# Performance work log

Measured on AMD Instinct MI355X. Metric: run time of the kernel, lower is better.

The kernel has to match this reference:

```python
import jax, jax.numpy as jnp
import numpy as np

B, N, DIN, HID, DOUT = 1024, 128, 256, 256, 256
KDIM = 4 * N  # fcq/fck output dim = n_node * 4


def setup_inputs() -> dict:
    key = jax.random.key(0)
    ks = jax.random.split(key, 11)
    s = 0.05
    x = jax.random.normal(ks[0], (B, N, DIN), dtype=jnp.float32)
    # binary attention mask in {0,1}
    mask = jax.random.randint(ks[1], (B, N, N), 0, 2).astype(jnp.float32)
    Wv = jax.random.normal(ks[2], (DIN, HID), dtype=jnp.float32) * s
    bv = jax.random.normal(ks[3], (HID,), dtype=jnp.float32) * s
    Wq = jax.random.normal(ks[4], (DIN, KDIM), dtype=jnp.float32) * s
    bq = jax.random.normal(ks[5], (KDIM,), dtype=jnp.float32) * s
    Wk = jax.random.normal(ks[6], (DIN, KDIM), dtype=jnp.float32) * s
    bk = jax.random.normal(ks[7], (KDIM,), dtype=jnp.float32) * s
    Wo = jax.random.normal(ks[8], (HID, DOUT), dtype=jnp.float32) * s
    bo = jax.random.normal(ks[9], (DOUT,), dtype=jnp.float32) * s
    return {"x": x, "mask": mask, "Wv": Wv, "bv": bv, "Wq": Wq, "bq": bq,
            "Wk": Wk, "bk": bk, "Wo": Wo, "bo": bo}


def reference(x, mask, Wv, bv, Wq, bq, Wk, bk, Wo, bo):
    # v: [B,N,HID], q/k: [B,N,4N]
    v = jax.nn.relu(jnp.einsum('bnd,dh->bnh', x, Wv) + bv)
    q = jax.nn.relu(jnp.einsum('bnd,dk->bnk', x, Wq) + bq)
    k = jax.nn.relu(jnp.einsum('bnd,dk->bnk', x, Wk) + bk)
    # scores: bmm(q, k^T) -> [B,N,N]
    scores = jnp.einsum('bnk,bmk->bnm', q, k)
    val = scores * mask - 1000.0 * (1.0 - mask)
    att = jax.nn.softmax(val, axis=2)
    ctx = jnp.einsum('bnm,bmh->bnh', att, v)  # [B,N,HID]
    out = jax.nn.relu(jnp.einsum('bnh,hd->bnd', ctx, Wo) + bo)
    return out, att
```

## Files before the change

kernel.cpp:

```cpp
#include <hip/hip_runtime.h>
#include <cstdint>
#include <cstddef>

#define B_SZ 1024
#define N_SZ 128
#define DIN 256
#define HID 256
#define DOUT 256
#define KD 512

typedef unsigned short u16;
typedef _Float16 f16x8 __attribute__((ext_vector_type(8)));
typedef float floatx4 __attribute__((ext_vector_type(4)));
typedef unsigned short u16x8 __attribute__((ext_vector_type(8)));

#define MFMA16(a,b,c) __builtin_amdgcn_mfma_f32_16x16x32_f16(a, b, c, 0, 0, 0)

__device__ __forceinline__ u16 f2h(float f) {
    _Float16 h = (_Float16)f;
    return *(u16*)&h;
}

__device__ __forceinline__ void barx() {
    asm volatile("" ::: "memory");
    __builtin_amdgcn_s_barrier();
    asm volatile("" ::: "memory");
}
__device__ __forceinline__ void bar_lgkm() {
    asm volatile("s_waitcnt lgkmcnt(0)" ::: "memory");
    __builtin_amdgcn_s_barrier();
    asm volatile("" ::: "memory");
}

#define XS_OFF  0
#define QS_OFF  65536
#define KS_OFF  81920
#define ATT_OFF 65536
#define WD_OFF  98304
#define RED_OFF 98304

__global__ __launch_bounds__(512, 2)
void fused_att(const float* __restrict__ x,   const float* __restrict__ mask,
               const u16* __restrict__ Wq_t,  const float* __restrict__ bq,
               const u16* __restrict__ Wk_t,  const float* __restrict__ bk,
               const u16* __restrict__ Wv_t,  const float* __restrict__ bv,
               const u16* __restrict__ Wo_t,  const float* __restrict__ bo,
               float* __restrict__ out,       float* __restrict__ att)
{
    __shared__ char LD[131072];

    const int tid  = threadIdx.x;
    const int wid  = tid >> 6;
    const int lane = tid & 63;
    const int l16  = lane & 15;
    const int quad = lane >> 4;
    const int b    = blockIdx.x;

    const int swm = (wid >> 2) * 64;
    const int swn = (wid & 3) * 32;
    const int qm0 = (wid >> 1) * 32;
    const int qn0 = (wid & 1) * 32;

    const int srow  = tid >> 3;
    const int sg    = tid & 7;
    const int swz16 = (sg * 16) ^ ((srow & 7) << 4);

    auto waddr = [&](const u16* Wb, int ch) -> const u16x8* {
        int kdv = ch >> 2, kcv = ch & 3;
        return (const u16x8*)(Wb + ((size_t)(kdv * 64) + srow) * DIN + kcv * 64 + sg * 8);
    };
    auto stage_writeQK = [&](int buf, u16x8 q8, u16x8 k8) {
        char* base = LD + WD_OFF + buf * 16384 + srow * 128 + swz16;
        *(u16x8*)base          = q8;
        *(u16x8*)(base + 8192) = k8;
    };
    auto load256 = [&](const u16* Wb, int kc, u16x8* r4) {
#pragma unroll
        for (int p = 0; p < 4; ++p)
            r4[p] = *(const u16x8*)(Wb + (size_t)(p * 64 + srow) * DIN + kc * 64 + sg * 8);
    };
    auto stage_write256 = [&](const u16x8* r4) {
#pragma unroll
        for (int p = 0; p < 4; ++p)
            *(u16x8*)(LD + WD_OFF + (p * 64 + srow) * 128 + swz16) = r4[p];
    };

    u16x8 rq[2], rk[2];
    rq[0] = *waddr(Wq_t, 0); rk[0] = *waddr(Wk_t, 0);
    rq[1] = *waddr(Wq_t, 1); rk[1] = *waddr(Wk_t, 1);

    {
        const float* xb = x + (size_t)b * (N_SZ * DIN);
        int row = tid >> 2;
        int c0  = (tid & 3) * 64;
        int sw  = (row & 7) << 4;
        const float* xr = xb + (size_t)row * DIN;
#pragma unroll
        for (int u = 0; u < 8; ++u) {
            int col = c0 + u * 8;
            float4 f0 = *(const float4*)(xr + col);
            float4 f1 = *(const float4*)(xr + col + 4);
            u16x8 o;
            o[0] = f2h(f0.x); o[1] = f2h(f0.y); o[2] = f2h(f0.z); o[3] = f2h(f0.w);
            o[4] = f2h(f1.x); o[5] = f2h(f1.y); o[6] = f2h(f1.z); o[7] = f2h(f1.w);
            *(u16x8*)(LD + ((row * 512 + col * 2) ^ sw)) = o;
        }
    }
    stage_writeQK(0, rq[0], rk[0]);
    bar_lgkm();

    f16x8 xa[2][8];
#pragma unroll
    for (int i = 0; i < 2; ++i)
#pragma unroll
        for (int t = 0; t < 8; ++t) {
            int r = qm0 + i * 16 + l16;
            int kofs = t * 32 + quad * 8;
            xa[i][t] = *(const f16x8*)(LD + ((r * 512 + kofs * 2) ^ ((r & 7) << 4)));
        }

    floatx4 sacc[4][2];
#pragma unroll
    for (int i = 0; i < 4; i++)
#pragma unroll
        for (int j = 0; j < 2; j++) sacc[i][j] = floatx4{0.f, 0.f, 0.f, 0.f};

    for (int kd = 0; kd < 8; ++kd) {
        float bqv[2], bkv[2];
#pragma unroll
        for (int j = 0; j < 2; j++) {
            int col = kd * 64 + qn0 + j * 16 + l16;
            bqv[j] = bq[col];
            bkv[j] = bk[col];
        }
        floatx4 qa[2][2], ka[2][2];
#pragma unroll
        for (int i = 0; i < 2; i++)
#pragma unroll
            for (int j = 0; j < 2; j++) {
                qa[i][j] = floatx4{0.f, 0.f, 0.f, 0.f};
                ka[i][j] = floatx4{0.f, 0.f, 0.f, 0.f};
            }

#pragma unroll
        for (int kc = 0; kc < 4; ++kc) {
            const int ch  = kd * 4 + kc;
            const int par = kc & 1;
            if (ch + 2 < 32) {
                rq[par] = *waddr(Wq_t, ch + 2);
                rk[par] = *waddr(Wk_t, ch + 2);
            }
            const char* WQ = LD + WD_OFF + par * 16384;
            const char* WK = WQ + 8192;
            __builtin_amdgcn_s_setprio(1);
#pragma unroll
            for (int ks = 0; ks < 2; ++ks) {
                f16x8 qf[2], kf[2];
#pragma unroll
                for (int j = 0; j < 2; ++j) {
                    int n  = qn0 + j * 16 + l16;
                    int by = (n * 128) + (((ks * 32 + quad * 8) * 2) ^ ((n & 7) << 4));
                    qf[j] = *(const f16x8*)(WQ + by);
                    kf[j] = *(const f16x8*)(WK + by);
                }
#pragma unroll
                for (int i = 0; i < 2; i++)
#pragma unroll
                    for (int j = 0; j < 2; j++) {
                        qa[i][j] = MFMA16(xa[i][kc * 2 + ks], qf[j], qa[i][j]);
                        ka[i][j] = MFMA16(xa[i][kc * 2 + ks], kf[j], ka[i][j]);
                    }
            }
            __builtin_amdgcn_s_setprio(0);
            if (ch + 1 < 32) stage_writeQK(par ^ 1, rq[par ^ 1], rk[par ^ 1]);
            bar_lgkm();
        }

#pragma unroll
        for (int i = 0; i < 2; i++)
#pragma unroll
            for (int j = 0; j < 2; j++)
#pragma unroll
                for (int r = 0; r < 4; r++) {
                    int rw_ = qm0 + i * 16 + quad * 4 + r;
                    int cl  = qn0 + j * 16 + l16;
                    int by  = (rw_ * 128) + ((cl * 2) ^ ((rw_ & 7) << 4));
                    *(u16*)(LD + QS_OFF + by) = f2h(fmaxf(qa[i][j][r] + bqv[j], 0.f));
                    *(u16*)(LD + KS_OFF + by) = f2h(fmaxf(ka[i][j][r] + bkv[j], 0.f));
                }
        bar_lgkm();

        __builtin_amdgcn_s_setprio(1);
#pragma unroll
        for (int ks = 0; ks < 2; ++ks) {
            f16x8 saf[4], sbf[2];
            int kb2 = (ks * 32 + quad * 8) * 2;
#pragma unroll
            for (int i = 0; i < 4; i++) {
                int r = swm + i * 16 + l16;
                saf[i] = *(const f16x8*)(LD + QS_OFF + (r * 128) + (kb2 ^ ((r & 7) << 4)));
            }
#pragma unroll
            for (int j = 0; j < 2; j++) {
                int n = swn + j * 16 + l16;
                sbf[j] = *(const f16x8*)(LD + KS_OFF + (n * 128) + (kb2 ^ ((n & 7) << 4)));
            }
#pragma unroll
            for (int i = 0; i < 4; i++)
#pragma unroll
                for (int j = 0; j < 2; j++)
                    sacc[i][j] = MFMA16(saf[i], sbf[j], sacc[i][j]);
        }
        __builtin_amdgcn_s_setprio(0);
    }

    u16x8 rw[4];
    load256(Wv_t, 0, rw);
    {
        const float* mb = mask + (size_t)b * (N_SZ * N_SZ);
        float mreg[4][4][2];
#pragma unroll
        for (int i = 0; i < 4; i++)
#pragma unroll
            for (int r = 0; r < 4; r++) {
                int row = swm + i * 16 + quad * 4 + r;
#pragma unroll
                for (int j = 0; j < 2; j++)
                    mreg[i][r][j] = mb[row * N_SZ + swn + j * 16 + l16];
            }

        float* REDm = (float*)(LD + RED_OFF);
        float* REDs = REDm + 512;
        float rmax[4][4];
#pragma unroll
        for (int i = 0; i < 4; i++) {
#pragma unroll
            for (int r = 0; r < 4; r++) {
                float mx = -1e30f;
#pragma unroll
                for (int j = 0; j < 2; j++) {
                    float mval = mreg[i][r][j];
                    float val  = sacc[i][j][r] * mval - 1000.f * (1.f - mval);
                    sacc[i][j][r] = val;
                    mx = fmaxf(mx, val);
                }
#pragma unroll
                for (int s = 1; s < 16; s <<= 1) mx = fmaxf(mx, __shfl_xor(mx, s, 64));
                rmax[i][r] = mx;
            }
        }
        if (l16 == 0) {
#pragma unroll
            for (int i = 0; i < 4; i++)
#pragma unroll
                for (int r = 0; r < 4; r++)
                    REDm[(wid & 3) * 128 + swm + i * 16 + quad * 4 + r] = rmax[i][r];
        }
        bar_lgkm();
#pragma unroll
        for (int i = 0; i < 4; i++)
#pragma unroll
            for (int r = 0; r < 4; r++) {
                int row = swm + i * 16 + quad * 4 + r;
                rmax[i][r] = fmaxf(fmaxf(REDm[row], REDm[128 + row]),
                                   fmaxf(REDm[256 + row], REDm[384 + row]));
            }

        float rsum[4][4];
#pragma unroll
        for (int i = 0; i < 4; i++) {
#pragma unroll
            for (int r = 0; r < 4; r++) {
                float s = 0.f;
#pragma unroll
                for (int j = 0; j < 2; j++) {
                    float e = __expf(sacc[i][j][r] - rmax[i][r]);
                    sacc[i][j][r] = e;
                    s += e;
                }
#pragma unroll
                for (int t = 1; t < 16; t <<= 1) s += __shfl_xor(s, t, 64);
                rsum[i][r] = s;
            }
        }
        if (l16 == 0) {
#pragma unroll
            for (int i = 0; i < 4; i++)
#pragma unroll
                for (int r = 0; r < 4; r++)
                    REDs[(wid & 3) * 128 + swm + i * 16 + quad * 4 + r] = rsum[i][r];
        }
        bar_lgkm();

        float* ao = att + (size_t)b * (N_SZ * N_SZ);
#pragma unroll
        for (int i = 0; i < 4; i++) {
#pragma unroll
            for (int r = 0; r < 4; r++) {
                int row = swm + i * 16 + quad * 4 + r;
                float inv = 1.f / (REDs[row] + REDs[128 + row] +
                                   REDs[256 + row] + REDs[384 + row]);
#pragma unroll
                for (int j = 0; j < 2; j++) {
                    int col = swn + j * 16 + l16;
                    float a = sacc[i][j][r] * inv;
                    ao[row * N_SZ + col] = a;
                    int by = (row * 256) + ((col * 2) ^ ((row & 7) << 4));
                    *(u16*)(LD + ATT_OFF + by) = f2h(a);
                }
            }
        }
        bar_lgkm();
    }

    floatx4 ctxa[4][4];
#pragma unroll
    for (int i = 0; i < 4; i++)
#pragma unroll
        for (int j = 0; j < 4; j++) ctxa[i][j] = floatx4{0.f, 0.f, 0.f, 0.f};

    {
        floatx4 va[4][4];
#pragma unroll
        for (int i = 0; i < 4; i++)
#pragma unroll
            for (int j = 0; j < 4; j++) va[i][j] = floatx4{0.f, 0.f, 0.f, 0.f};

#pragma unroll
        for (int kc = 0; kc < 4; ++kc) {
            stage_write256(rw);
            if (kc < 3) load256(Wv_t, kc + 1, rw);
            else        load256(Wo_t, 0, rw);
            bar_lgkm();
            __builtin_amdgcn_s_setprio(1);
#pragma unroll
            for (int ks = 0; ks < 2; ++ks) {
                int kofs = kc * 64 + ks * 32 + quad * 8;
                f16x8 af[4], wf[4];
#pragma unroll
                for (int i = 0; i < 4; i++) {
                    int r = swm + i * 16 + l16;
                    af[i] = *(const f16x8*)(LD + ((r * 512 + kofs * 2) ^ ((r & 7) << 4)));
                }
#pragma unroll
                for (int jj = 0; jj < 4; jj++) {
                    int n = (jj >> 1) * 128 + swn + (jj & 1) * 16 + l16;
                    wf[jj] = *(const f16x8*)(LD + WD_OFF + (n * 128) +
                                             (((ks * 32 + quad * 8) * 2) ^ ((n & 7) << 4)));
                }
#pragma unroll
                for (int i = 0; i < 4; i++)
#pragma unroll
                    for (int jj = 0; jj < 4; jj++)
                        va[i][jj] = MFMA16(af[i], wf[jj], va[i][jj]);
            }
            __builtin_amdgcn_s_setprio(0);
            barx();
        }

        float bvv[4];
#pragma unroll
        for (int jj = 0; jj < 4; jj++)
            bvv[jj] = bv[(jj >> 1) * 128 + swn + (jj & 1) * 16 + l16];
#pragma unroll
        for (int i = 0; i < 4; i++)
#pragma unroll
            for (int jj = 0; jj < 4; jj++)
#pragma unroll
                for (int r = 0; r < 4; r++) {
                    int m = swm + i * 16 + quad * 4 + r;
                    int h = (jj >> 1) * 128 + swn + (jj & 1) * 16 + l16;
                    int by = (h * 256) + ((m * 2) ^ ((h & 7) << 4));
                    *(u16*)(LD + by) = f2h(fmaxf(va[i][jj][r] + bvv[jj], 0.f));
                }
        bar_lgkm();

        __builtin_amdgcn_s_setprio(1);
#pragma unroll
        for (int ks = 0; ks < 4; ++ks) {
            int kb2 = (ks * 32 + quad * 8) * 2;
            f16x8 paf[4], pbf[4];
#pragma unroll
            for (int i = 0; i < 4; i++) {
                int r = swm + i * 16 + l16;
                paf[i] = *(const f16x8*)(LD + ATT_OFF + (r * 256) + (kb2 ^ ((r & 7) << 4)));
            }
#pragma unroll
            for (int jj = 0; jj < 4; jj++) {
                int h = (jj >> 1) * 128 + swn + (jj & 1) * 16 + l16;
                pbf[jj] = *(const f16x8*)(LD + (h * 256) + (kb2 ^ ((h & 7) << 4)));
            }
#pragma unroll
            for (int i = 0; i < 4; i++)
#pragma unroll
                for (int jj = 0; jj < 4; jj++)
                    ctxa[i][jj] = MFMA16(paf[i], pbf[jj], ctxa[i][jj]);
        }
        __builtin_amdgcn_s_setprio(0);
        barx();
    }

#pragma unroll
    for (int i = 0; i < 4; i++)
#pragma unroll
        for (int jj = 0; jj < 4; jj++)
#pragma unroll
            for (int r = 0; r < 4; r++) {
                int row = swm + i * 16 + quad * 4 + r;
                int col = (jj >> 1) * 128 + swn + (jj & 1) * 16 + l16;
                int by  = (row * 512) + ((col * 2) ^ ((row & 7) << 4));
                *(u16*)(LD + by) = f2h(ctxa[i][jj][r]);
            }
    bar_lgkm();

    {
        floatx4 oa[4][4];
#pragma unroll
        for (int i = 0; i < 4; i++)
#pragma unroll
            for (int j = 0; j < 4; j++) oa[i][j] = floatx4{0.f, 0.f, 0.f, 0.f};

#pragma unroll
        for (int kc = 0; kc < 4; ++kc) {
            stage_write256(rw);
            if (kc < 3) load256(Wo_t, kc + 1, rw);
            bar_lgkm();
            __builtin_amdgcn_s_setprio(1);
#pragma unroll
            for (int ks = 0; ks < 2; ++ks) {
                int kofs = kc * 64 + ks * 32 + quad * 8;
                f16x8 caf[4], wof[4];
#pragma unroll
                for (int i = 0; i < 4; i++) {
                    int r = swm + i * 16 + l16;
                    caf[i] = *(const f16x8*)(LD + ((r * 512 + kofs * 2) ^ ((r & 7) << 4)));
                }
#pragma unroll
                for (int jj = 0; jj < 4; jj++) {
                    int n = (jj >> 1) * 128 + swn + (jj & 1) * 16 + l16;
                    wof[jj] = *(const f16x8*)(LD + WD_OFF + (n * 128) +
                                              (((ks * 32 + quad * 8) * 2) ^ ((n & 7) << 4)));
                }
#pragma unroll
                for (int i = 0; i < 4; i++)
#pragma unroll
                    for (int jj = 0; jj < 4; jj++)
                        oa[i][jj] = MFMA16(caf[i], wof[jj], oa[i][jj]);
            }
            __builtin_amdgcn_s_setprio(0);
            if (kc < 3) barx();
        }

        float* ob = out + (size_t)b * (N_SZ * DOUT);
        float bov[4];
#pragma unroll
        for (int jj = 0; jj < 4; jj++)
            bov[jj] = bo[(jj >> 1) * 128 + swn + (jj & 1) * 16 + l16];
#pragma unroll
        for (int i = 0; i < 4; i++)
#pragma unroll
            for (int jj = 0; jj < 4; jj++)
#pragma unroll
                for (int r = 0; r < 4; r++) {
                    int row = swm + i * 16 + quad * 4 + r;
                    int col = (jj >> 1) * 128 + swn + (jj & 1) * 16 + l16;
                    ob[(size_t)row * DOUT + col] = fmaxf(oa[i][jj][r] + bov[jj], 0.f);
                }
    }
}

__global__ __launch_bounds__(256)
void wtrans(const float* __restrict__ W, u16* __restrict__ Wt, int K, int Nc)
{
    int idx = blockIdx.x * 256 + threadIdx.x;
    if (idx < K * Nc) {
        int k = idx / Nc, n = idx % Nc;
        Wt[(size_t)n * K + k] = f2h(W[idx]);
    }
}

extern "C" void kernel_launch(void* const* d_in, const int* in_sizes, int n_in,
                              void* d_out, int out_size, void* d_ws, size_t ws_size,
                              hipStream_t stream)
{
    const float* x    = (const float*)d_in[0];
    const float* mask = (const float*)d_in[1];
    const float* Wv   = (const float*)d_in[2];
    const float* bv   = (const float*)d_in[3];
    const float* Wq   = (const float*)d_in[4];
    const float* bq   = (const float*)d_in[5];
    const float* Wk   = (const float*)d_in[6];
    const float* bk   = (const float*)d_in[7];
    const float* Wo   = (const float*)d_in[8];
    const float* bo   = (const float*)d_in[9];

    float* out = (float*)d_out;
    float* att = out + (size_t)B_SZ * N_SZ * DOUT;

    char* ws = (char*)d_ws;
    u16* Wq_t = (u16*)ws;
    u16* Wk_t = Wq_t + (size_t)KD * DIN;
    u16* Wv_t = Wk_t + (size_t)KD * DIN;
    u16* Wo_t = Wv_t + (size_t)HID * DIN;

    wtrans<<<(DIN * KD + 255) / 256, 256, 0, stream>>>(Wq, Wq_t, DIN, KD);
    wtrans<<<(DIN * KD + 255) / 256, 256, 0, stream>>>(Wk, Wk_t, DIN, KD);
    wtrans<<<(DIN * HID + 255) / 256, 256, 0, stream>>>(Wv, Wv_t, DIN, HID);
    wtrans<<<(HID * DOUT + 255) / 256, 256, 0, stream>>>(Wo, Wo_t, HID, DOUT);

    fused_att<<<B_SZ, 512, 0, stream>>>(x, mask,
                                        Wq_t, bq, Wk_t, bk, Wv_t, bv, Wo_t, bo,
                                        out, att);

    (void)in_sizes; (void)n_in; (void)out_size; (void)ws_size;
}
```

Baseline: 475.2 us.

## Process four batches per persistent block with cross-batch prefetch of x and weights

Each workgroup now loops over four batch elements instead of one, launching B/4 blocks. While the current batch's output projection finishes, it prefetches the next batch's x tile and first Q/K weight chunks, and it loads the mask early during the last score step. The four weight-transpose launches are merged into one kernel. The aim is to hide global load latency and cut launch and block-startup overhead. The cost is 256 blocks on a GPU with many CUs, which gives worse occupancy and tail balance, and more register pressure from the prefetch buffers.

```diff
diff --git a/kernel.cpp b/kernel.cpp
--- a/kernel.cpp
+++ b/kernel.cpp
@@ -13,6 +13,7 @@
 typedef _Float16 f16x8 __attribute__((ext_vector_type(8)));
 typedef float floatx4 __attribute__((ext_vector_type(4)));
 typedef unsigned short u16x8 __attribute__((ext_vector_type(8)));
+typedef unsigned short u16x4 __attribute__((ext_vector_type(4)));
 
 #define MFMA16(a,b,c) __builtin_amdgcn_mfma_f32_16x16x32_f16(a, b, c, 0, 0, 0)
 
@@ -54,7 +55,6 @@
     const int lane = tid & 63;
     const int l16  = lane & 15;
     const int quad = lane >> 4;
-    const int b    = blockIdx.x;
 
     const int swm = (wid >> 2) * 64;
     const int swn = (wid & 3) * 32;
@@ -85,377 +85,336 @@
             *(u16x8*)(LD + WD_OFF + (p * 64 + srow) * 128 + swz16) = r4[p];
     };
 
-    u16x8 rq[2], rk[2];
-    rq[0] = *waddr(Wq_t, 0); rk[0] = *waddr(Wk_t, 0);
-    rq[1] = *waddr(Wq_t, 1); rk[1] = *waddr(Wk_t, 1);
-
-    {
-        const float* xb = x + (size_t)b * (N_SZ * DIN);
-        int row = tid >> 2;
-        int c0  = (tid & 3) * 64;
-        int sw  = (row & 7) << 4;
-        const float* xr = xb + (size_t)row * DIN;
+    const int xrow = tid >> 2;
+    const int xc0  = (tid & 3) * 64;
+    auto x_load = [&](const float* xb, float4* xr16) {
+        const float* xr = xb + (size_t)xrow * DIN + xc0;
+#pragma unroll
+        for (int u = 0; u < 16; ++u) xr16[u] = *(const float4*)(xr + u * 4);
+    };
+    auto x_store = [&](const float4* xr16) {
+        int sw = (xrow & 7) << 4;
 #pragma unroll
         for (int u = 0; u < 8; ++u) {
-            int col = c0 + u * 8;
-            float4 f0 = *(const float4*)(xr + col);
-            float4 f1 = *(const float4*)(xr + col + 4);
+            int col = xc0 + u * 8;
+            float4 f0 = xr16[2 * u], f1 = xr16[2 * u + 1];
             u16x8 o;
             o[0] = f2h(f0.x); o[1] = f2h(f0.y); o[2] = f2h(f0.z); o[3] = f2h(f0.w);
             o[4] = f2h(f1.x); o[5] = f2h(f1.y); o[6] = f2h(f1.z); o[7] = f2h(f1.w);
-            *(u16x8*)(LD + ((row * 512 + col * 2) ^ sw)) = o;
+            *(u16x8*)(LD + ((xrow * 512 + col * 2) ^ sw)) = o;
         }
-    }
+    };
+
+    u16x8 rq[2], rk[2];
+    float4 xr16[16];
+    x_load(x + (size_t)(blockIdx.x * 4) * (N_SZ * DIN), xr16);
+    rq[0] = *waddr(Wq_t, 0); rk[0] = *waddr(Wk_t, 0);
+    rq[1] = *waddr(Wq_t, 1); rk[1] = *waddr(Wk_t, 1);
+    x_store(xr16);
     stage_writeQK(0, rq[0], rk[0]);
     bar_lgkm();
 
-    f16x8 xa[2][8];
-#pragma unroll
-    for (int i = 0; i < 2; ++i)
-#pragma unroll
-        for (int t = 0; t < 8; ++t) {
-            int r = qm0 + i * 16 + l16;
-            int kofs = t * 32 + quad * 8;
-            xa[i][t] = *(const f16x8*)(LD + ((r * 512 + kofs * 2) ^ ((r & 7) << 4)));
+#pragma unroll 1
+    for (int ib = 0; ib < 4; ++ib) {
+        const int b = blockIdx.x * 4 + ib;
+
+        f16x8 xa[2][8];
+#pragma unroll
+        for (int i = 0; i < 2; ++i)
+#pragma unroll
+            for (int t = 0; t < 8; ++t) {
+                int r = qm0 + i * 16 + l16;
+                int kofs = t * 32 + quad * 8;
+                xa[i][t] = *(const f16x8*)(LD + ((r * 512 + kofs * 2) ^ ((r & 7) << 4)));
+            }
+
+        floatx4 sacc[4][2];
+#pragma unroll
+        for (int i = 0; i < 4; i++)
+#pragma unroll
+            for (int j = 0; j < 2; j++) sacc[i][j] = floatx4{0.f, 0.f, 0.f, 0.f};
+
+        float mreg[4][4][2];
+        const float* mb = mask + (size_t)b * (N_SZ * N_SZ);
+
+#pragma unroll 1
+        for (int kd = 0; kd < 8; ++kd) {
+            float bqv[2], bkv[2];
+#pragma unroll
+            for (int j = 0; j < 2; j++) {
+                int col = kd * 64 + qn0 + j * 16 + l16;
+                bqv[j] = bq[col];
+                bkv[j] = bk[col];
+            }
+            floatx4 qa[2][2], ka[2][2];
+#pragma unroll
+            for (int i = 0; i < 2; i++)
+#pragma unroll
+                for (int j = 0; j < 2; j++) {
+                    qa[i][j] = floatx4{0.f, 0.f, 0.f, 0.f};
+                    ka[i][j] = floatx4{0.f, 0.f, 0.f, 0.f};
+                }
+
+#pragma unroll
+            for (int kc = 0; kc < 4; ++kc) {
+                const int ch  = kd * 4 + kc;
+                const int par = kc & 1;
+                if (ch + 2 < 32) {
+                    rq[par] = *waddr(Wq_t, ch + 2);
+                    rk[par] = *waddr(Wk_t, ch + 2);
+                }
+                const char* WQ = LD + WD_OFF + par * 16384;
+                const char* WK = WQ + 8192;
+                __builtin_amdgcn_s_setprio(1);
+#pragma unroll
+                for (int ks = 0; ks < 2; ++ks) {
+                    f16x8 qf[2], kf[2];
+#pragma unroll
+                    for (int j = 0; j < 2; ++j) {
+                        int n  = qn0 + j * 16 + l16;
+                        int by = (n * 128) + (((ks * 32 + quad * 8) * 2) ^ ((n & 7) << 4));
+                        qf[j] = *(const f16x8*)(WQ + by);
+                        kf[j] = *(const f16x8*)(WK + by);
+                    }
+#pragma unroll
+                    for (int i = 0; i < 2; i++)
+#pragma unroll
+                        for (int j = 0; j < 2; j++) {
+                            qa[i][j] = MFMA16(xa[i][kc * 2 + ks], qf[j], qa[i][j]);
+                            ka[i][j] = MFMA16(xa[i][kc * 2 + ks], kf[j], ka[i][j]);
+                        }
+                }
+                __builtin_amdgcn_s_setprio(0);
+                if (ch + 1 < 32) stage_writeQK(par ^ 1, rq[par ^ 1], rk[par ^ 1]);
+                bar_lgkm();
+            }
+
+#pragma unroll
+            for (int i = 0; i < 2; i++)
+#pragma unroll
+                for (int j = 0; j < 2; j++)
+#pragma unroll
+                    for (int r = 0; r < 4; r++) {
+                        int rw_ = qm0 + i * 16 + quad * 4 + r;
+                        int cl  = qn0 + j * 16 + l16;
+                        int by  = (rw_ * 128) + ((cl * 2) ^ ((rw_ & 7) << 4));
+                        *(u16*)(LD + QS_OFF + by) = f2h(fmaxf(qa[i][j][r] + bqv[j], 0.f));
+                        *(u16*)(LD + KS_OFF + by) = f2h(fmaxf(ka[i][j][r] + bkv[j], 0.f));
+                    }
+            bar_lgkm();
+
+            if (kd == 7) {
+#pragma unroll
+                for (int i = 0; i < 4; i++)
+#pragma unroll
+                    for (int r = 0; r < 4; r++) {
+                        int row = swm + i * 16 + quad * 4 + r;
+#pragma unroll
+                        for (int j = 0; j < 2; j++)
+                            mreg[i][r][j] = mb[row * N_SZ + swn + j * 16 + l16];
+                    }
+            }
+
+            __builtin_amdgcn_s_setprio(1);
+#pragma unroll
+            for (int ks = 0; ks < 2; ++ks) {
+                f16x8 saf[4], sbf[2];
+                int kb2 = (ks * 32 + quad * 8) * 2;
+#pragma unroll
+                for (int i = 0; i < 4; i++) {
+                    int r = swm + i * 16 + l16;
+                    saf[i] = *(const f16x8*)(LD + QS_OFF + (r * 128) + (kb2 ^ ((r & 7) << 4)));
+                }
+#pragma unroll
+                for (int j = 0; j < 2; j++) {
+                    int n = swn + j * 16 + l16;
+                    sbf[j] = *(const f16x8*)(LD + KS_OFF + (n * 128) + (kb2 ^ ((n & 7) << 4)));
+                }
+#pragma unroll
+                for (int i = 0; i < 4; i++)
+#pragma unroll
+                    for (int j = 0; j < 2; j++)
+                        sacc[i][j] = MFMA16(saf[i], sbf[j], sacc[i][j]);
+            }
+            __builtin_amdgcn_s_setprio(0);
         }
 
-    floatx4 sacc[4][2];
-#pragma unroll
-    for (int i = 0; i < 4; i++)
-#pragma unroll
-        for (int j = 0; j < 2; j++) sacc[i][j] = floatx4{0.f, 0.f, 0.f, 0.f};
-
-    for (int kd = 0; kd < 8; ++kd) {
-        float bqv[2], bkv[2];
-#pragma unroll
-        for (int j = 0; j < 2; j++) {
-            int col = kd * 64 + qn0 + j * 16 + l16;
-            bqv[j] = bq[col];
-            bkv[j] = bk[col];
-        }
-        floatx4 qa[2][2], ka[2][2];
-#pragma unroll
-        for (int i = 0; i < 2; i++)
-#pragma unroll
-            for (int j = 0; j < 2; j++) {
-                qa[i][j] = floatx4{0.f, 0.f, 0.f, 0.f};
-                ka[i][j] = floatx4{0.f, 0.f, 0.f, 0.f};
-            }
-
-#pragma unroll
-        for (int kc = 0; kc < 4; ++kc) {
-            const int ch  = kd * 4 + kc;
-            const int par = kc & 1;
-            if (ch + 2 < 32) {
-                rq[par] = *waddr(Wq_t, ch + 2);
-                rk[par] = *waddr(Wk_t, ch + 2);
-            }
-            const char* WQ = LD + WD_OFF + par * 16384;
-            const char* WK = WQ + 8192;
-            __builtin_amdgcn_s_setprio(1);
-#pragma unroll
-            for (int ks = 0; ks < 2; ++ks) {
-                f16x8 qf[2], kf[2];
-#pragma unroll
-                for (int j = 0; j < 2; ++j) {
-                    int n  = qn0 + j * 16 + l16;
-                    int by = (n * 128) + (((ks * 32 + quad * 8) * 2) ^ ((n & 7) << 4));
-                    qf[j] = *(const f16x8*)(WQ + by);
-                    kf[j] = *(const f16x8*)(WK + by);
-                }
-#pragma unroll
-                for (int i = 0; i < 2; i++)
+        u16x8 rw[4];
+        load256(Wv_t, 0, rw);
+        {
+            float* REDm = (float*)(LD + RED_OFF);
+            float* REDs = REDm + 512;
+            float rmax[4][4];
+#pragma unroll
+            for (int i = 0; i < 4; i++) {
+#pragma unroll
+                for (int r = 0; r < 4; r++) {
+                    float mx = -1e30f;
 #pragma unroll
                     for (int j = 0; j < 2; j++) {
-                        qa[i][j] = MFMA16(xa[i][kc * 2 + ks], qf[j], qa[i][j]);
-                        ka[i][j] = MFMA16(xa[i][kc * 2 + ks], kf[j], ka[i][j]);
-                    }
-            }
-            __builtin_amdgcn_s_setprio(0);
-            if (ch + 1 < 32) stage_writeQK(par ^ 1, rq[par ^ 1], rk[par ^ 1]);
+                        float mval = mreg[i][r][j];
+                        float val  = sacc[i][j][r] * mval - 1000.f * (1.f - mval);
+                        sacc[i][j][r] = val;
+                        mx = fmaxf(mx, val);
+                    }
+#pragma unroll
+                    for (int s = 1; s < 16; s <<= 1) mx = fmaxf(mx, __shfl_xor(mx, s, 64));
+                    rmax[i][r] = mx;
+                }
+            }
+            if (l16 == 0) {
+#pragma unroll
+                for (int i = 0; i < 4; i++)
+#pragma unroll
+                    for (int r = 0; r < 4; r++)
+                        REDm[(wid & 3) * 128 + swm + i * 16 + quad * 4 + r] = rmax[i][r];
+            }
+            bar_lgkm();
+#pragma unroll
+            for (int i = 0; i < 4; i++)
+#pragma unroll
+                for (int r = 0; r < 4; r++) {
+                    int row = swm + i * 16 + quad * 4 + r;
+                    rmax[i][r] = fmaxf(fmaxf(REDm[row], REDm[128 + row]),
+                                       fmaxf(REDm[256 + row], REDm[384 + row]));
+                }
+
+            float rsum[4][4];
+#pragma unroll
+            for (int i = 0; i < 4; i++) {
+#pragma unroll
+                for (int r = 0; r < 4; r++) {
+                    float s = 0.f;
+#pragma unroll
+                    for (int j = 0; j < 2; j++) {
+                        float e = __expf(sacc[i][j][r] - rmax[i][r]);
+                        sacc[i][j][r] = e;
+                        s += e;
+                    }
+#pragma unroll
+                    for (int t = 1; t < 16; t <<= 1) s += __shfl_xor(s, t, 64);
+                    rsum[i][r] = s;
+                }
+            }
+            if (l16 == 0) {
+#pragma unroll
+                for (int i = 0; i < 4; i++)
+#pragma unroll
+                    for (int r = 0; r < 4; r++)
+                        REDs[(wid & 3) * 128 + swm + i * 16 + quad * 4 + r] = rsum[i][r];
+            }
+            bar_lgkm();
+
+            float* ao = att + (size_t)b * (N_SZ * N_SZ);
+#pragma unroll
+            for (int i = 0; i < 4; i++) {
+#pragma unroll
+                for (int r = 0; r < 4; r++) {
+                    int row = swm + i * 16 + quad * 4 + r;
+                    float inv = 1.f / (REDs[row] + REDs[128 + row] +
+                                       REDs[256 + row] + REDs[384 + row]);
+#pragma unroll
+                    for (int j = 0; j < 2; j++) {
+                        int col = swn + j * 16 + l16;
+                        float a = sacc[i][j][r] * inv;
+                        ao[row * N_SZ + col] = a;
+                        int by = (row * 256) + ((col * 2) ^ ((row & 7) << 4));
+                        *(u16*)(LD + ATT_OFF + by) = f2h(a);
+                    }
+                }
+            }
             bar_lgkm();
         }
 
-#pragma unroll
-        for (int i = 0; i < 2; i++)
-#pragma unroll
-            for (int j = 0; j < 2; j++)
-#pragma unroll
-                for (int r = 0; r < 4; r++) {
-                    int rw_ = qm0 + i * 16 + quad * 4 + r;
-                    int cl  = qn0 + j * 16 + l16;
-                    int by  = (rw_ * 128) + ((cl * 2) ^ ((rw_ & 7) << 4));
-                    *(u16*)(LD + QS_OFF + by) = f2h(fmaxf(qa[i][j][r] + bqv[j], 0.f));
-                    *(u16*)(LD + KS_OFF + by) = f2h(fmaxf(ka[i][j][r] + bkv[j], 0.f));
-                }
-        bar_lgkm();
-
-        __builtin_amdgcn_s_setprio(1);
-#pragma unroll
-        for (int ks = 0; ks < 2; ++ks) {
-            f16x8 saf[4], sbf[2];
-            int kb2 = (ks * 32 + quad * 8) * 2;
-#pragma unroll
-            for (int i = 0; i < 4; i++) {
-                int r = swm + i * 16 + l16;
-                saf[i] = *(const f16x8*)(LD + QS_OFF + (r * 128) + (kb2 ^ ((r & 7) << 4)));
-            }
-#pragma unroll
-            for (int j = 0; j < 2; j++) {
-                int n = swn + j * 16 + l16;
-                sbf[j] = *(const f16x8*)(LD + KS_OFF + (n * 128) + (kb2 ^ ((n & 7) << 4)));
-            }
+        floatx4 ctxa[4][4];
+#pragma unroll
+        for (int i = 0; i < 4; i++)
+#pragma unroll
+            for (int j = 0; j < 4; j++) ctxa[i][j] = floatx4{0.f, 0.f, 0.f, 0.f};
+
+        {
+            floatx4 va[4][4];
 #pragma unroll
             for (int i = 0; i < 4; i++)
 #pragma unroll
-                for (int j = 0; j < 2; j++)
-                    sacc[i][j] = MFMA16(saf[i], sbf[j], sacc[i][j]);
-        }
-        __builtin_amdgcn_s_setprio(0);
-    }
-
-    u16x8 rw[4];
-    load256(Wv_t, 0, rw);
-    {
-        const float* mb = mask + (size_t)b * (N_SZ * N_SZ);
-        float mreg[4][4][2];
-#pragma unroll
-        for (int i = 0; i < 4; i++)
-#pragma unroll
-            for (int r = 0; r < 4; r++) {
-                int row = swm + i * 16 + quad * 4 + r;
-#pragma unroll
-                for (int j = 0; j < 2; j++)
-                    mreg[i][r][j] = mb[row * N_SZ + swn + j * 16 + l16];
-            }
-
-        float* REDm = (float*)(LD + RED_OFF);
-        float* REDs = REDm + 512;
-        float rmax[4][4];
-#pragma unroll
-        for (int i = 0; i < 4; i++) {
-#pragma unroll
-            for (int r = 0; r < 4; r++) {
-                float mx = -1e30f;
-#pragma unroll
-                for (int j = 0; j < 2; j++) {
-                    float mval = mreg[i][r][j];
-                    float val  = sacc[i][j][r] * mval - 1000.f * (1.f - mval);
-                    sacc[i][j][r] = val;
-                    mx = fmaxf(mx, val);
-                }
-#pragma unroll
-                for (int s = 1; s < 16; s <<= 1) mx = fmaxf(mx, __shfl_xor(mx, s, 64));
-                rmax[i][r] = mx;
-            }
-        }
-        if (l16 == 0) {
+                for (int j = 0; j < 4; j++) va[i][j] = floatx4{0.f, 0.f, 0.f, 0.f};
+
+#pragma unroll
+            for (int kc = 0; kc < 4; ++kc) {
+                stage_write256(rw);
+                if (kc < 3) load256(Wv_t, kc + 1, rw);
+                else        load256(Wo_t, 0, rw);
+                bar_lgkm();
+                __builtin_amdgcn_s_setprio(1);
+#pragma unroll
+                for (int ks = 0; ks < 2; ++ks) {
+                    int kofs = kc * 64 + ks * 32 + quad * 8;
+                    f16x8 af[4], wf[4];
+#pragma unroll
+                    for (int i = 0; i < 4; i++) {
+                        int r = swm + i * 16 + l16;
+                        af[i] = *(const f16x8*)(LD + ((r * 512 + kofs * 2) ^ ((r & 7) << 4)));
+                    }
+#pragma unroll
+                    for (int jj = 0; jj < 4; jj++) {
+                        int n = (jj >> 1) * 128 + swn + (jj & 1) * 16 + l16;
+                        wf[jj] = *(const f16x8*)(LD + WD_OFF + (n * 128) +
+                                                 (((ks * 32 + quad * 8) * 2) ^ ((n & 7) << 4)));
+                    }
+#pragma unroll
+                    for (int i = 0; i < 4; i++)
+#pragma unroll
+                        for (int jj = 0; jj < 4; jj++)
+                            va[i][jj] = MFMA16(af[i], wf[jj], va[i][jj]);
+                }
+                __builtin_amdgcn_s_setprio(0);
+                barx();
+            }
+
+            float bvv[4];
+#pragma unroll
+            for (int jj = 0; jj < 4; jj++)
+                bvv[jj] = bv[(jj >> 1) * 128 + swn + (jj & 1) * 16 + l16];
 #pragma unroll
             for (int i = 0; i < 4; i++)
 #pragma unroll
-                for (int r = 0; r < 4; r++)
-                    REDm[(wid & 3) * 128 + swm + i * 16 + quad * 4 + r] = rmax[i][r];
-        }
-        bar_lgkm();
-#pragma unroll
-        for (int i = 0; i < 4; i++)
-#pragma unroll
-            for (int r = 0; r < 4; r++) {
-                int row = swm + i * 16 + quad * 4 + r;
-                rmax[i][r] = fmaxf(fmaxf(REDm[row], REDm[128 + row]),
-                                   fmaxf(REDm[256 + row], REDm[384 + row]));
-            }
-
-        float rsum[4][4];
-#pragma unroll
-        for (int i = 0; i < 4; i++) {
-#pragma unroll
-            for (int r = 0; r < 4; r++) {
-                float s = 0.f;
-#pragma unroll
-                for (int j = 0; j < 2; j++) {
-                    float e = __expf(sacc[i][j][r] - rmax[i][r]);
-                    sacc[i][j][r] = e;
-                    s += e;
-                }
-#pragma unroll
-                for (int t = 1; t < 16; t <<= 1) s += __shfl_xor(s, t, 64);
-                rsum[i][r] = s;
-            }
-        }
-        if (l16 == 0) {
-#pragma unroll
-            for (int i = 0; i < 4; i++)
-#pragma unroll
-                for (int r = 0; r < 4; r++)
-                    REDs[(wid & 3) * 128 + swm + i * 16 + quad * 4 + r] = rsum[i][r];
-        }
-        bar_lgkm();
-
-        float* ao = att + (size_t)b * (N_SZ * N_SZ);
-#pragma unroll
-        for (int i = 0; i < 4; i++) {
-#pragma unroll
-            for (int r = 0; r < 4; r++) {
-                int row = swm + i * 16 + quad * 4 + r;
-                float inv = 1.f / (REDs[row] + REDs[128 + row] +
-                                   REDs[256 + row] + REDs[384 + row]);
-#pragma unroll
-                for (int j = 0; j < 2; j++) {
-                    int col = swn + j * 16 + l16;
-                    float a = sacc[i][j][r] * inv;
-                    ao[row * N_SZ + col] = a;
-                    int by = (row * 256) + ((col * 2) ^ ((row & 7) << 4));
-                    *(u16*)(LD + ATT_OFF + by) = f2h(a);
-                }
-            }
-        }
-        bar_lgkm();
-    }
-
-    floatx4 ctxa[4][4];
-#pragma unroll
-    for (int i = 0; i < 4; i++)
-#pragma unroll
-        for (int j = 0; j < 4; j++) ctxa[i][j] = floatx4{0.f, 0.f, 0.f, 0.f};
-
-    {
-        floatx4 va[4][4];
-#pragma unroll
-        for (int i = 0; i < 4; i++)
-#pragma unroll
-            for (int j = 0; j < 4; j++) va[i][j] = floatx4{0.f, 0.f, 0.f, 0.f};
-
-#pragma unroll
-        for (int kc = 0; kc < 4; ++kc) {
-            stage_write256(rw);
-            if (kc < 3) load256(Wv_t, kc + 1, rw);
-            else        load256(Wo_t, 0, rw);
+                for (int jj = 0; jj < 4; jj++) {
+                    int m0 = swm + i * 16 + quad * 4;
+                    int h  = (jj >> 1) * 128 + swn + (jj & 1) * 16 + l16;
+                    u16x4 pk;
+#pragma unroll
+                    for (int r = 0; r < 4; r++)
+                        pk[r] = f2h(fmaxf(va[i][jj][r] + bvv[jj], 0.f));
+                    int by = (h * 256) + ((m0 * 2) ^ ((h & 7) << 4));
+                    *(u16x4*)(LD + by) = pk;
+                }
             bar_lgkm();
+
             __builtin_amdgcn_s_setprio(1);
 #pragma unroll
-            for (int ks = 0; ks < 2; ++ks) {
-                int kofs = kc * 64 + ks * 32 + quad * 8;
-                f16x8 af[4], wf[4];
+            for (int ks = 0; ks < 4; ++ks) {
+                int kb2 = (ks * 32 + quad * 8) * 2;
+                f16x8 paf[4], pbf[4];
 #pragma unroll
                 for (int i = 0; i < 4; i++) {
                     int r = swm + i * 16 + l16;
-                    af[i] = *(const f16x8*)(LD + ((r * 512 + kofs * 2) ^ ((r & 7) << 4)));
+                    paf[i] = *(const f16x8*)(LD + ATT_OFF + (r * 256) + (kb2 ^ ((r & 7) << 4)));
                 }
 #pragma unroll
                 for (int jj = 0; jj < 4; jj++) {
-                    int n = (jj >> 1) * 128 + swn + (jj & 1) * 16 + l16;
-                    wf[jj] = *(const f16x8*)(LD + WD_OFF + (n * 128) +
-                                             (((ks * 32 + quad * 8) * 2) ^ ((n & 7) << 4)));
+                    int h = (jj >> 1) * 128 + swn + (jj & 1) * 16 + l16;
+                    pbf[jj] = *(const f16x8*)(LD + (h * 256) + (kb2 ^ ((h & 7) << 4)));
                 }
 #pragma unroll
                 for (int i = 0; i < 4; i++)
 #pragma unroll
                     for (int jj = 0; jj < 4; jj++)
-                        va[i][jj] = MFMA16(af[i], wf[jj], va[i][jj]);
+                        ctxa[i][jj] = MFMA16(paf[i], pbf[jj], ctxa[i][jj]);
             }
             __builtin_amdgcn_s_setprio(0);
             barx();
         }
 
-        float bvv[4];
-#pragma unroll
-        for (int jj = 0; jj < 4; jj++)
-            bvv[jj] = bv[(jj >> 1) * 128 + swn + (jj & 1) * 16 + l16];
-#pragma unroll
-        for (int i = 0; i < 4; i++)
-#pragma unroll
-            for (int jj = 0; jj < 4; jj++)
-#pragma unroll
-                for (int r = 0; r < 4; r++) {
-                    int m = swm + i * 16 + quad * 4 + r;
-                    int h = (jj >> 1) * 128 + swn + (jj & 1) * 16 + l16;
-                    int by = (h * 256) + ((m * 2) ^ ((h & 7) << 4));
-                    *(u16*)(LD + by) = f2h(fmaxf(va[i][jj][r] + bvv[jj], 0.f));
-                }
-        bar_lgkm();
-
-        __builtin_amdgcn_s_setprio(1);
-#pragma unroll
-        for (int ks = 0; ks < 4; ++ks) {
-            int kb2 = (ks * 32 + quad * 8) * 2;
-            f16x8 paf[4], pbf[4];
-#pragma unroll
-            for (int i = 0; i < 4; i++) {
-                int r = swm + i * 16 + l16;
-                paf[i] = *(const f16x8*)(LD + ATT_OFF + (r * 256) + (kb2 ^ ((r & 7) << 4)));
-            }
-#pragma unroll
-            for (int jj = 0; jj < 4; jj++) {
-                int h = (jj >> 1) * 128 + swn + (jj & 1) * 16 + l16;
-                pbf[jj] = *(const f16x8*)(LD + (h * 256) + (kb2 ^ ((h & 7) << 4)));
-            }
-#pragma unroll
-            for (int i = 0; i < 4; i++)
-#pragma unroll
-                for (int jj = 0; jj < 4; jj++)
-                    ctxa[i][jj] = MFMA16(paf[i], pbf[jj], ctxa[i][jj]);
-        }
-        __builtin_amdgcn_s_setprio(0);
-        barx();
-    }
-
-#pragma unroll
-    for (int i = 0; i < 4; i++)
-#pragma unroll
-        for (int jj = 0; jj < 4; jj++)
-#pragma unroll
-            for (int r = 0; r < 4; r++) {
-                int row = swm + i * 16 + quad * 4 + r;
-                int col = (jj >> 1) * 128 + swn + (jj & 1) * 16 + l16;
-                int by  = (row * 512) + ((col * 2) ^ ((row & 7) << 4));
-                *(u16*)(LD + by) = f2h(ctxa[i][jj][r]);
-            }
-    bar_lgkm();
-
-    {
-        floatx4 oa[4][4];
-#pragma unroll
-        for (int i = 0; i < 4; i++)
-#pragma unroll
-            for (int j = 0; j < 4; j++) oa[i][j] = floatx4{0.f, 0.f, 0.f, 0.f};
-
-#pragma unroll
-        for (int kc = 0; kc < 4; ++kc) {
-            stage_write256(rw);
-            if (kc < 3) load256(Wo_t, kc + 1, rw);
-            bar_lgkm();
-            __builtin_amdgcn_s_setprio(1);
-#pragma unroll
-            for (int ks = 0; ks < 2; ++ks) {
-                int kofs = kc * 64 + ks * 32 + quad * 8;
-                f16x8 caf[4], wof[4];
-#pragma unroll
-                for (int i = 0; i < 4; i++) {
-                    int r = swm + i * 16 + l16;
-                    caf[i] = *(const f16x8*)(LD + ((r * 512 + kofs * 2) ^ ((r & 7) << 4)));
-                }
-#pragma unroll
-                for (int jj = 0; jj < 4; jj++) {
-                    int n = (jj >> 1) * 128 + swn + (jj & 1) * 16 + l16;
-                    wof[jj] = *(const f16x8*)(LD + WD_OFF + (n * 128) +
-                                              (((ks * 32 + quad * 8) * 2) ^ ((n & 7) << 4)));
-                }
-#pragma unroll
-                for (int i = 0; i < 4; i++)
-#pragma unroll
-                    for (int jj = 0; jj < 4; jj++)
-                        oa[i][jj] = MFMA16(caf[i], wof[jj], oa[i][jj]);
-            }
-            __builtin_amdgcn_s_setprio(0);
-            if (kc < 3) barx();
-        }
-
-        float* ob = out + (size_t)b * (N_SZ * DOUT);
-        float bov[4];
-#pragma unroll
-        for (int jj = 0; jj < 4; jj++)
-            bov[jj] = bo[(jj >> 1) * 128 + swn + (jj & 1) * 16 + l16];
 #pragma unroll
         for (int i = 0; i < 4; i++)
 #pragma unroll
@@ -464,18 +423,105 @@
                 for (int r = 0; r < 4; r++) {
                     int row = swm + i * 16 + quad * 4 + r;
                     int col = (jj >> 1) * 128 + swn + (jj & 1) * 16 + l16;
-                    ob[(size_t)row * DOUT + col] = fmaxf(oa[i][jj][r] + bov[jj], 0.f);
-                }
+                    int by  = (row * 512) + ((col * 2) ^ ((row & 7) << 4));
+                    *(u16*)(LD + by) = f2h(ctxa[i][jj][r]);
+                }
+        bar_lgkm();
+
+        {
+            floatx4 oa[4][4];
+#pragma unroll
+            for (int i = 0; i < 4; i++)
+#pragma unroll
+                for (int j = 0; j < 4; j++) oa[i][j] = floatx4{0.f, 0.f, 0.f, 0.f};
+
+#pragma unroll
+            for (int kc = 0; kc < 4; ++kc) {
+                stage_write256(rw);
+                if (kc < 3) load256(Wo_t, kc + 1, rw);
+                bar_lgkm();
+                __builtin_amdgcn_s_setprio(1);
+#pragma unroll
+                for (int ks = 0; ks < 2; ++ks) {
+                    int kofs = kc * 64 + ks * 32 + quad * 8;
+                    f16x8 caf[4], wof[4];
+#pragma unroll
+                    for (int i = 0; i < 4; i++) {
+                        int r = swm + i * 16 + l16;
+                        caf[i] = *(const f16x8*)(LD + ((r * 512 + kofs * 2) ^ ((r & 7) << 4)));
+                    }
+#pragma unroll
+                    for (int jj = 0; jj < 4; jj++) {
+                        int n = (jj >> 1) * 128 + swn + (jj & 1) * 16 + l16;
+                        wof[jj] = *(const f16x8*)(LD + WD_OFF + (n * 128) +
+                                                  (((ks * 32 + quad * 8) * 2) ^ ((n & 7) << 4)));
+                    }
+#pragma unroll
+                    for (int i = 0; i < 4; i++)
+#pragma unroll
+                        for (int jj = 0; jj < 4; jj++)
+                            oa[i][jj] = MFMA16(caf[i], wof[jj], oa[i][jj]);
+                }
+                __builtin_amdgcn_s_setprio(0);
+                if (kc < 3) barx();
+            }
+
+            if (ib < 3) {
+                x_load(x + (size_t)(b + 1) * (N_SZ * DIN), xr16);
+                rq[0] = *waddr(Wq_t, 0); rk[0] = *waddr(Wk_t, 0);
+                rq[1] = *waddr(Wq_t, 1); rk[1] = *waddr(Wk_t, 1);
+            }
+
+            float* ob = out + (size_t)b * (N_SZ * DOUT);
+            float bov[4];
+#pragma unroll
+            for (int jj = 0; jj < 4; jj++)
+                bov[jj] = bo[(jj >> 1) * 128 + swn + (jj & 1) * 16 + l16];
+#pragma unroll
+            for (int i = 0; i < 4; i++)
+#pragma unroll
+                for (int jj = 0; jj < 4; jj++)
+#pragma unroll
+                    for (int r = 0; r < 4; r++) {
+                        int row = swm + i * 16 + quad * 4 + r;
+                        int col = (jj >> 1) * 128 + swn + (jj & 1) * 16 + l16;
+                        ob[(size_t)row * DOUT + col] = fmaxf(oa[i][jj][r] + bov[jj], 0.f);
+                    }
+        }
+
+        if (ib < 3) {
+            barx();
+            x_store(xr16);
+            stage_writeQK(0, rq[0], rk[0]);
+            bar_lgkm();
+        }
     }
 }
 
+#define SQK (DIN * KD)
+#define SVO (DIN * HID)
 __global__ __launch_bounds__(256)
-void wtrans(const float* __restrict__ W, u16* __restrict__ Wt, int K, int Nc)
+void wtrans_all(const float* __restrict__ Wq, const float* __restrict__ Wk,
+                const float* __restrict__ Wv, const float* __restrict__ Wo,
+                u16* __restrict__ Wq_t, u16* __restrict__ Wk_t,
+                u16* __restrict__ Wv_t, u16* __restrict__ Wo_t)
 {
     int idx = blockIdx.x * 256 + threadIdx.x;
-    if (idx < K * Nc) {
-        int k = idx / Nc, n = idx % Nc;
-        Wt[(size_t)n * K + k] = f2h(W[idx]);
+    if (idx < SQK) {
+        int k = idx / KD, n = idx % KD;
+        Wq_t[(size_t)n * DIN + k] = f2h(Wq[idx]);
+    } else if (idx < 2 * SQK) {
+        int i = idx - SQK;
+        int k = i / KD, n = i % KD;
+        Wk_t[(size_t)n * DIN + k] = f2h(Wk[i]);
+    } else if (idx < 2 * SQK + SVO) {
+        int i = idx - 2 * SQK;
+        int k = i / HID, n = i % HID;
+        Wv_t[(size_t)n * DIN + k] = f2h(Wv[i]);
+    } else if (idx < 2 * SQK + 2 * SVO) {
+        int i = idx - 2 * SQK - SVO;
+        int k = i / DOUT, n = i % DOUT;
+        Wo_t[(size_t)n * HID + k] = f2h(Wo[i]);
     }
 }
 
@@ -503,14 +549,12 @@
     u16* Wv_t = Wk_t + (size_t)KD * DIN;
     u16* Wo_t = Wv_t + (size_t)HID * DIN;
 
-    wtrans<<<(DIN * KD + 255) / 256, 256, 0, stream>>>(Wq, Wq_t, DIN, KD);
-    wtrans<<<(DIN * KD + 255) / 256, 256, 0, stream>>>(Wk, Wk_t, DIN, KD);
-    wtrans<<<(DIN * HID + 255) / 256, 256, 0, stream>>>(Wv, Wv_t, DIN, HID);
-    wtrans<<<(HID * DOUT + 255) / 256, 256, 0, stream>>>(Wo, Wo_t, HID, DOUT);
-
-    fused_att<<<B_SZ, 512, 0, stream>>>(x, mask,
-                                        Wq_t, bq, Wk_t, bk, Wv_t, bv, Wo_t, bo,
-                                        out, att);
+    wtrans_all<<<(2 * SQK + 2 * SVO + 255) / 256, 256, 0, stream>>>(
+        Wq, Wk, Wv, Wo, Wq_t, Wk_t, Wv_t, Wo_t);
+
+    fused_att<<<B_SZ / 4, 512, 0, stream>>>(x, mask,
+                                            Wq_t, bq, Wk_t, bk, Wv_t, bv, Wo_t, bo,
+                                            out, att);
 
     (void)in_sizes; (void)n_in; (void)out_size; (void)ws_size;
 }
```

Result: slower. 882.9 us (+85.8%).
